# Kernel tuning notes

Hardware: AMD Instinct MI355X
Metric: run time of the kernel (lower is better)

The kernel has to match this reference:

```python
import jax, jax.numpy as jnp
import numpy as np

NUM_CLASSES = 1000
FEAT_DIM = 256
BATCH = 8192
MARGIN = 5.0
ALPHA = 1.0
BETA = 1.0


def setup_inputs() -> dict:
    key = jax.random.key(0)
    k1, k2, k3 = jax.random.split(key, 3)
    x = jax.random.normal(k1, (BATCH, FEAT_DIM), dtype=jnp.float32)
    labels = jax.random.randint(k2, (BATCH,), 0, NUM_CLASSES, dtype=jnp.int64)
    centers = jax.random.normal(k3, (NUM_CLASSES, FEAT_DIM), dtype=jnp.float32)
    return {"x": x, "labels": labels, "centers": centers}


def reference(x, labels, centers):
    # --- intra-class part ---
    # distmat_intra[i, j] = ||x_i||^2 + ||x_j||^2 - 2 x_i . x_j  (then relu + sqrt)
    mag = jnp.sum(x * x, axis=1)                      # (B,)
    sim = x @ x.T                                     # (B, B)
    d2 = mag[None, :] + mag[:, None] - 2.0 * sim      # (B, B)
    d = jnp.sqrt(jax.nn.relu(d2))                     # (B, B)

    # mask[i, j] = labels[i] == labels[j]; original gathers masked values per row,
    # clamps to [1e-12, 1e12], sorts descending and uses only the top-2 values.
    mask = labels[:, None] == labels[None, :]         # (B, B) bool
    vals = jnp.where(mask, jnp.clip(d, 1e-12, 1e12), -jnp.inf)
    top2, _ = jax.lax.top_k(vals.reshape(-1), 2)      # two largest intra-class dists
    k = 2.0
    loss_intra = k / (1.0 / top2[0] + 1.0 / top2[1])  # harmonic mean * k

    # --- inter-class part (faithful to original broadcasting) ---
    # distmat_inter[i, j] = 2 ||c_j||^2 - 2 c_i . c_j
    cmag = 2.0 * jnp.sum(centers * centers, axis=1)   # (C,)
    inter = cmag[None, :] - 2.0 * (centers @ centers.T)
    inter = jnp.clip(inter.reshape(-1), 1e-12, 1e12)
    loss_inter = jnp.clip(MARGIN - jnp.min(inter), 0.0, 1e6)

    return ALPHA * loss_intra + BETA * loss_inter
```

## Files before the change

kernel.cpp:

```cpp
#include <hip/hip_runtime.h>
#include <math.h>

#define BATCH 8192
#define FEAT  256
#define NCLS  1000

#define NGEMM  136
#define REPL   4
#define NINTRA (REPL*NCLS)
#define NBLK   (NGEMM + NINTRA)
#define ROWCAP 16
#define MEMCAP 96


__global__ __launch_bounds__(256) void k_main(const float* __restrict__ x,
                                              const int* __restrict__ labels,
                                              const float* __restrict__ centers,
                                              float* __restrict__ ws) {
    __shared__ __align__(16) char raw[18944];
    __shared__ float wred[4];
    __shared__ int cnt;
    int t = threadIdx.x;
    int lane = t & 63, w = t >> 6;

    if (blockIdx.x < NGEMM) {
        float (*As)[36] = reinterpret_cast<float(*)[36]>(raw);
        float (*Bs)[36] = reinterpret_cast<float(*)[36]>(raw + 9216);
        float* cmagI    = reinterpret_cast<float*>(raw + 18432);
        float* cmagJ    = reinterpret_cast<float*>(raw + 18688);

        int bi = 0, rem = blockIdx.x;
        while (rem >= 16 - bi) { rem -= 16 - bi; ++bi; }
        int bj = bi + rem;
        int i0 = bi * 64, j0 = bj * 64;

        for (int q = w; q < 64; q += 4) {
            int gi = i0 + q, gj = j0 + q;
            float sI = 0.0f, sJ = 0.0f;
            if (gi < NCLS) {
                float4 v = reinterpret_cast<const float4*>(centers + (size_t)gi * FEAT)[lane];
                sI = v.x * v.x + v.y * v.y + v.z * v.z + v.w * v.w;
            }
            if (gj < NCLS) {
                float4 v = reinterpret_cast<const float4*>(centers + (size_t)gj * FEAT)[lane];
                sJ = v.x * v.x + v.y * v.y + v.z * v.z + v.w * v.w;
            }
            #pragma unroll
            for (int o = 32; o > 0; o >>= 1) {
                sI += __shfl_xor(sI, o);
                sJ += __shfl_xor(sJ, o);
            }
            if (lane == 0) { cmagI[q] = 2.0f * sI; cmagJ[q] = 2.0f * sJ; }
        }

        int tx = t & 15, ty = t >> 4;
        float acc[4][4] = {{0.f}};
        for (int kk = 0; kk < FEAT; kk += 32) {
            #pragma unroll
            for (int e = t; e < 512; e += 256) {
                int row = e >> 3, q = e & 7;
                int col = kk + q * 4;
                int gi = i0 + row, gj = j0 + row;
                float4 av = (gi < NCLS)
                    ? *reinterpret_cast<const float4*>(centers + (size_t)gi * FEAT + col)
                    : make_float4(0.f, 0.f, 0.f, 0.f);
                float4 bv = (gj < NCLS)
                    ? *reinterpret_cast<const float4*>(centers + (size_t)gj * FEAT + col)
                    : make_float4(0.f, 0.f, 0.f, 0.f);
                *reinterpret_cast<float4*>(&As[row][q * 4]) = av;
                *reinterpret_cast<float4*>(&Bs[row][q * 4]) = bv;
            }
            __syncthreads();
            #pragma unroll
            for (int kc = 0; kc < 32; kc += 4) {
                float a[4][4], b[4][4];
                #pragma unroll
                for (int ii = 0; ii < 4; ++ii) {
                    float4 v = *reinterpret_cast<float4*>(&As[ty * 4 + ii][kc]);
                    a[ii][0] = v.x; a[ii][1] = v.y; a[ii][2] = v.z; a[ii][3] = v.w;
                }
                #pragma unroll
                for (int jj = 0; jj < 4; ++jj) {
                    float4 v = *reinterpret_cast<float4*>(&Bs[tx * 4 + jj][kc]);
                    b[jj][0] = v.x; b[jj][1] = v.y; b[jj][2] = v.z; b[jj][3] = v.w;
                }
                #pragma unroll
                for (int kq = 0; kq < 4; ++kq)
                    #pragma unroll
                    for (int ii = 0; ii < 4; ++ii)
                        #pragma unroll
                        for (int jj = 0; jj < 4; ++jj)
                            acc[ii][jj] += a[ii][kq] * b[jj][kq];
            }
            __syncthreads();
        }
        float lmin = 1e30f;
        #pragma unroll
        for (int jj = 0; jj < 4; ++jj) {
            int J = j0 + tx * 4 + jj;
            #pragma unroll
            for (int ii = 0; ii < 4; ++ii) {
                int I = i0 + ty * 4 + ii;
                if (I < NCLS && J < NCLS) {
                    float v1 = cmagJ[tx * 4 + jj] - 2.0f * acc[ii][jj];
                    v1 = fminf(fmaxf(v1, 1e-12f), 1e12f);
                    float v2 = cmagI[ty * 4 + ii] - 2.0f * acc[ii][jj];
                    v2 = fminf(fmaxf(v2, 1e-12f), 1e12f);
                    lmin = fminf(lmin, fminf(v1, v2));
                }
            }
        }
        #pragma unroll
        for (int o = 32; o > 0; o >>= 1) lmin = fminf(lmin, __shfl_xor(lmin, o));
        if (lane == 0) wred[w] = lmin;
        __syncthreads();
        if (t == 0) {
            float m = fminf(fminf(wred[0], wred[1]), fminf(wred[2], wred[3]));
            ws[blockIdx.x] = m;
        }
    } else {
        int bid = blockIdx.x - NGEMM;
        int c   = bid >> 2;
        int r   = bid & 3;
        float (*rowS)[256] = reinterpret_cast<float(*)[256]>(raw);
        int*   mem  = reinterpret_cast<int*>(raw + 16384);
        float* magS = reinterpret_cast<float*>(raw + 16768);

        if (t == 0) cnt = 0;
        __syncthreads();
        const int4* gl4 = reinterpret_cast<const int4*>(labels);
        #pragma unroll
        for (int k = 0; k < 8; ++k) {
            int4 lv = gl4[t + (k << 8)];
            int base = (t + (k << 8)) << 2;
            if (lv.x == c) { int p = atomicAdd(&cnt, 1); if (p < MEMCAP) mem[p] = base;     }
            if (lv.y == c) { int p = atomicAdd(&cnt, 1); if (p < MEMCAP) mem[p] = base + 1; }
            if (lv.z == c) { int p = atomicAdd(&cnt, 1); if (p < MEMCAP) mem[p] = base + 2; }
            if (lv.w == c) { int p = atomicAdd(&cnt, 1); if (p < MEMCAP) mem[p] = base + 3; }
        }
        __syncthreads();
        int n = cnt < MEMCAP ? cnt : MEMCAP;
        float vmax = 0.0f;
        if (n >= 2) {
            const float4* x4 = reinterpret_cast<const float4*>(x);
            for (int m = w; m < n; m += 4) {
                int row = mem[m];
                float4 v = x4[(size_t)row * 64 + lane];
                if (m < ROWCAP)
                    *reinterpret_cast<float4*>(&rowS[m][lane << 2]) = v;
                float s = v.x * v.x + v.y * v.y + v.z * v.z + v.w * v.w;
                #pragma unroll
                for (int o = 32; o > 0; o >>= 1) s += __shfl_xor(s, o);
                if (lane == 0) magS[m] = s;
            }
            __syncthreads();
            int npairs = n * (n - 1) / 2;
            for (int p = r * 4 + w; p < npairs; p += 16) {
                int a = 0, rem = p;
                while (rem >= n - 1 - a) { rem -= n - 1 - a; ++a; }
                int b = a + 1 + rem;
                float4 va = (a < ROWCAP)
                    ? *reinterpret_cast<float4*>(&rowS[a][lane << 2])
                    : x4[(size_t)mem[a] * 64 + lane];
                float4 vb = (b < ROWCAP)
                    ? *reinterpret_cast<float4*>(&rowS[b][lane << 2])
                    : x4[(size_t)mem[b] * 64 + lane];
                float s = va.x * vb.x + va.y * vb.y + va.z * vb.z + va.w * vb.w;
                #pragma unroll
                for (int o = 32; o > 0; o >>= 1) s += __shfl_xor(s, o);
                float d2 = magS[a] + magS[b] - 2.0f * s;
                float d  = sqrtf(fmaxf(d2, 0.0f));
                d = fminf(fmaxf(d, 1e-12f), 1e12f);
                vmax = fmaxf(vmax, d);
            }
        }
        if (lane == 0) wred[w] = vmax;
        __syncthreads();
        if (t == 0) {
            float m = fmaxf(fmaxf(wred[0], wred[1]), fmaxf(wred[2], wred[3]));
            ws[NGEMM + bid] = m;
        }
    }
}

__global__ __launch_bounds__(256) void k_final(const float* __restrict__ ws,
                                               float* __restrict__ out) {
    __shared__ float smx[4], smn[4];
    int t = threadIdx.x, lane = t & 63, w = t >> 6;
    float mn = 1e30f, mx = 0.0f;
    for (int i = t; i < NGEMM; i += 256)  mn = fminf(mn, ws[i]);
    for (int i = t; i < NINTRA; i += 256) mx = fmaxf(mx, ws[NGEMM + i]);
    #pragma unroll
    for (int o = 32; o > 0; o >>= 1) {
        mx = fmaxf(mx, __shfl_xor(mx, o));
        mn = fminf(mn, __shfl_xor(mn, o));
    }
    if (lane == 0) { smx[w] = mx; smn[w] = mn; }
    __syncthreads();
    if (t == 0) {
        mx = fmaxf(fmaxf(smx[0], smx[1]), fmaxf(smx[2], smx[3]));
        mn = fminf(fminf(smn[0], smn[1]), fminf(smn[2], smn[3]));
        float M = fmaxf(mx, 1e-12f);
        float r = 1.0f / M;
        float li2 = 2.0f / (r + r);
        float m = fminf(mn, 1e12f);
        float linter = fminf(fmaxf(5.0f - m, 0.0f), 1e6f);
        out[0] = li2 + linter;
    }
}

extern "C" void kernel_launch(void* const* d_in, const int* in_sizes, int n_in,
                              void* d_out, int out_size, void* d_ws, size_t ws_size,
                              hipStream_t stream) {
    const float* x       = (const float*)d_in[0];
    const int*   labels  = (const int*)d_in[1];
    const float* centers = (const float*)d_in[2];
    float*        ws     = (float*)d_ws;
    float*        out    = (float*)d_out;

    k_main<<<NBLK, 256, 0, stream>>>(x, labels, centers, ws);
    k_final<<<1, 256, 0, stream>>>(ws, out);
}
```

Baseline: 97.30 us.

## Shrink center-GEMM tiles to 32x32, halve intra replication, reorder block roles

The centers Gram GEMM now uses 32x32 tiles, which means 528 upper-triangular blocks instead of 136. Each thread computes a 2x2 output and loads are staged into a transposed shared-memory layout. Intra-class blocks now use 2 replicas per class instead of 4 and are placed first in the grid, with the GEMM blocks after them. The intent is to spread the GEMM across more CUs and cut redundant label scans in the intra blocks, at the cost of lower arithmetic intensity per GEMM block and more pair work per intra block.

```diff
diff --git a/kernel.cpp b/kernel.cpp
--- a/kernel.cpp
+++ b/kernel.cpp
@@ -5,123 +5,28 @@
 #define FEAT  256
 #define NCLS  1000
 
-#define NGEMM  136
-#define REPL   4
-#define NINTRA (REPL*NCLS)
-#define NBLK   (NGEMM + NINTRA)
-#define ROWCAP 16
-#define MEMCAP 96
+#define REPL    2
+#define NINTRA  (REPL*NCLS)
+#define NGEMM   528
+#define NBLK    (NINTRA + NGEMM)
+#define ROWCAP  16
+#define MEMCAP  96
 
 
 __global__ __launch_bounds__(256) void k_main(const float* __restrict__ x,
                                               const int* __restrict__ labels,
                                               const float* __restrict__ centers,
                                               float* __restrict__ ws) {
-    __shared__ __align__(16) char raw[18944];
+    __shared__ __align__(16) char raw[17152];
     __shared__ float wred[4];
     __shared__ int cnt;
     int t = threadIdx.x;
     int lane = t & 63, w = t >> 6;
 
-    if (blockIdx.x < NGEMM) {
-        float (*As)[36] = reinterpret_cast<float(*)[36]>(raw);
-        float (*Bs)[36] = reinterpret_cast<float(*)[36]>(raw + 9216);
-        float* cmagI    = reinterpret_cast<float*>(raw + 18432);
-        float* cmagJ    = reinterpret_cast<float*>(raw + 18688);
-
-        int bi = 0, rem = blockIdx.x;
-        while (rem >= 16 - bi) { rem -= 16 - bi; ++bi; }
-        int bj = bi + rem;
-        int i0 = bi * 64, j0 = bj * 64;
-
-        for (int q = w; q < 64; q += 4) {
-            int gi = i0 + q, gj = j0 + q;
-            float sI = 0.0f, sJ = 0.0f;
-            if (gi < NCLS) {
-                float4 v = reinterpret_cast<const float4*>(centers + (size_t)gi * FEAT)[lane];
-                sI = v.x * v.x + v.y * v.y + v.z * v.z + v.w * v.w;
-            }
-            if (gj < NCLS) {
-                float4 v = reinterpret_cast<const float4*>(centers + (size_t)gj * FEAT)[lane];
-                sJ = v.x * v.x + v.y * v.y + v.z * v.z + v.w * v.w;
-            }
-            #pragma unroll
-            for (int o = 32; o > 0; o >>= 1) {
-                sI += __shfl_xor(sI, o);
-                sJ += __shfl_xor(sJ, o);
-            }
-            if (lane == 0) { cmagI[q] = 2.0f * sI; cmagJ[q] = 2.0f * sJ; }
-        }
-
-        int tx = t & 15, ty = t >> 4;
-        float acc[4][4] = {{0.f}};
-        for (int kk = 0; kk < FEAT; kk += 32) {
-            #pragma unroll
-            for (int e = t; e < 512; e += 256) {
-                int row = e >> 3, q = e & 7;
-                int col = kk + q * 4;
-                int gi = i0 + row, gj = j0 + row;
-                float4 av = (gi < NCLS)
-                    ? *reinterpret_cast<const float4*>(centers + (size_t)gi * FEAT + col)
-                    : make_float4(0.f, 0.f, 0.f, 0.f);
-                float4 bv = (gj < NCLS)
-                    ? *reinterpret_cast<const float4*>(centers + (size_t)gj * FEAT + col)
-                    : make_float4(0.f, 0.f, 0.f, 0.f);
-                *reinterpret_cast<float4*>(&As[row][q * 4]) = av;
-                *reinterpret_cast<float4*>(&Bs[row][q * 4]) = bv;
-            }
-            __syncthreads();
-            #pragma unroll
-            for (int kc = 0; kc < 32; kc += 4) {
-                float a[4][4], b[4][4];
-                #pragma unroll
-                for (int ii = 0; ii < 4; ++ii) {
-                    float4 v = *reinterpret_cast<float4*>(&As[ty * 4 + ii][kc]);
-                    a[ii][0] = v.x; a[ii][1] = v.y; a[ii][2] = v.z; a[ii][3] = v.w;
-                }
-                #pragma unroll
-                for (int jj = 0; jj < 4; ++jj) {
-                    float4 v = *reinterpret_cast<float4*>(&Bs[tx * 4 + jj][kc]);
-                    b[jj][0] = v.x; b[jj][1] = v.y; b[jj][2] = v.z; b[jj][3] = v.w;
-                }
-                #pragma unroll
-                for (int kq = 0; kq < 4; ++kq)
-                    #pragma unroll
-                    for (int ii = 0; ii < 4; ++ii)
-                        #pragma unroll
-                        for (int jj = 0; jj < 4; ++jj)
-                            acc[ii][jj] += a[ii][kq] * b[jj][kq];
-            }
-            __syncthreads();
-        }
-        float lmin = 1e30f;
-        #pragma unroll
-        for (int jj = 0; jj < 4; ++jj) {
-            int J = j0 + tx * 4 + jj;
-            #pragma unroll
-            for (int ii = 0; ii < 4; ++ii) {
-                int I = i0 + ty * 4 + ii;
-                if (I < NCLS && J < NCLS) {
-                    float v1 = cmagJ[tx * 4 + jj] - 2.0f * acc[ii][jj];
-                    v1 = fminf(fmaxf(v1, 1e-12f), 1e12f);
-                    float v2 = cmagI[ty * 4 + ii] - 2.0f * acc[ii][jj];
-                    v2 = fminf(fmaxf(v2, 1e-12f), 1e12f);
-                    lmin = fminf(lmin, fminf(v1, v2));
-                }
-            }
-        }
-        #pragma unroll
-        for (int o = 32; o > 0; o >>= 1) lmin = fminf(lmin, __shfl_xor(lmin, o));
-        if (lane == 0) wred[w] = lmin;
-        __syncthreads();
-        if (t == 0) {
-            float m = fminf(fminf(wred[0], wred[1]), fminf(wred[2], wred[3]));
-            ws[blockIdx.x] = m;
-        }
-    } else {
-        int bid = blockIdx.x - NGEMM;
-        int c   = bid >> 2;
-        int r   = bid & 3;
+    if (blockIdx.x < NINTRA) {
+        int bid = blockIdx.x;
+        int c   = bid >> 1;
+        int r   = bid & 1;
         float (*rowS)[256] = reinterpret_cast<float(*)[256]>(raw);
         int*   mem  = reinterpret_cast<int*>(raw + 16384);
         float* magS = reinterpret_cast<float*>(raw + 16768);
@@ -155,7 +60,7 @@
             }
             __syncthreads();
             int npairs = n * (n - 1) / 2;
-            for (int p = r * 4 + w; p < npairs; p += 16) {
+            for (int p = r * 4 + w; p < npairs; p += 8) {
                 int a = 0, rem = p;
                 while (rem >= n - 1 - a) { rem -= n - 1 - a; ++a; }
                 int b = a + 1 + rem;
@@ -178,7 +83,89 @@
         __syncthreads();
         if (t == 0) {
             float m = fmaxf(fmaxf(wred[0], wred[1]), fmaxf(wred[2], wred[3]));
-            ws[NGEMM + bid] = m;
+            ws[bid] = m;
+        }
+    } else {
+        float (*As)[34] = reinterpret_cast<float(*)[34]>(raw);
+        float (*Bs)[34] = reinterpret_cast<float(*)[34]>(raw + 4352);
+        float* cmagI    = reinterpret_cast<float*>(raw + 8704);
+        float* cmagJ    = reinterpret_cast<float*>(raw + 8832);
+
+        int bi = 0, rem = blockIdx.x - NINTRA;
+        while (rem >= 32 - bi) { rem -= 32 - bi; ++bi; }
+        int bj = bi + rem;
+        int i0 = bi * 32, j0 = bj * 32;
+
+        for (int q = w; q < 32; q += 4) {
+            int gi = i0 + q, gj = j0 + q;
+            float sI = 0.0f, sJ = 0.0f;
+            if (gi < NCLS) {
+                float4 v = reinterpret_cast<const float4*>(centers + (size_t)gi * FEAT)[lane];
+                sI = v.x * v.x + v.y * v.y + v.z * v.z + v.w * v.w;
+            }
+            if (gj < NCLS) {
+                float4 v = reinterpret_cast<const float4*>(centers + (size_t)gj * FEAT)[lane];
+                sJ = v.x * v.x + v.y * v.y + v.z * v.z + v.w * v.w;
+            }
+            #pragma unroll
+            for (int o = 32; o > 0; o >>= 1) {
+                sI += __shfl_xor(sI, o);
+                sJ += __shfl_xor(sJ, o);
+            }
+            if (lane == 0) { cmagI[q] = 2.0f * sI; cmagJ[q] = 2.0f * sJ; }
+        }
+
+        int tx = t & 15, ty = t >> 4;
+        float acc[2][2] = {{0.f, 0.f}, {0.f, 0.f}};
+        for (int kk = 0; kk < FEAT; kk += 32) {
+            {
+                int row = t >> 3, q = t & 7;
+                int col = kk + q * 4;
+                int gi = i0 + row, gj = j0 + row;
+                float4 av = (gi < NCLS)
+                    ? *reinterpret_cast<const float4*>(centers + (size_t)gi * FEAT + col)
+                    : make_float4(0.f, 0.f, 0.f, 0.f);
+                float4 bv = (gj < NCLS)
+                    ? *reinterpret_cast<const float4*>(centers + (size_t)gj * FEAT + col)
+                    : make_float4(0.f, 0.f, 0.f, 0.f);
+                As[q * 4 + 0][row] = av.x; As[q * 4 + 1][row] = av.y;
+                As[q * 4 + 2][row] = av.z; As[q * 4 + 3][row] = av.w;
+                Bs[q * 4 + 0][row] = bv.x; Bs[q * 4 + 1][row] = bv.y;
+                Bs[q * 4 + 2][row] = bv.z; Bs[q * 4 + 3][row] = bv.w;
+            }
+            __syncthreads();
+            #pragma unroll
+            for (int k = 0; k < 32; ++k) {
+                float2 a2 = *reinterpret_cast<float2*>(&As[k][ty * 2]);
+                float2 b2 = *reinterpret_cast<float2*>(&Bs[k][tx * 2]);
+                acc[0][0] += a2.x * b2.x; acc[0][1] += a2.x * b2.y;
+                acc[1][0] += a2.y * b2.x; acc[1][1] += a2.y * b2.y;
+            }
+            __syncthreads();
+        }
+        float lmin = 1e30f;
+        #pragma unroll
+        for (int jj = 0; jj < 2; ++jj) {
+            int J = j0 + tx * 2 + jj;
+            #pragma unroll
+            for (int ii = 0; ii < 2; ++ii) {
+                int I = i0 + ty * 2 + ii;
+                if (I < NCLS && J < NCLS) {
+                    float v1 = cmagJ[tx * 2 + jj] - 2.0f * acc[ii][jj];
+                    v1 = fminf(fmaxf(v1, 1e-12f), 1e12f);
+                    float v2 = cmagI[ty * 2 + ii] - 2.0f * acc[ii][jj];
+                    v2 = fminf(fmaxf(v2, 1e-12f), 1e12f);
+                    lmin = fminf(lmin, fminf(v1, v2));
+                }
+            }
+        }
+        #pragma unroll
+        for (int o = 32; o > 0; o >>= 1) lmin = fminf(lmin, __shfl_xor(lmin, o));
+        if (lane == 0) wred[w] = lmin;
+        __syncthreads();
+        if (t == 0) {
+            float m = fminf(fminf(wred[0], wred[1]), fminf(wred[2], wred[3]));
+            ws[blockIdx.x] = m;
         }
     }
 }
@@ -188,8 +175,8 @@
     __shared__ float smx[4], smn[4];
     int t = threadIdx.x, lane = t & 63, w = t >> 6;
     float mn = 1e30f, mx = 0.0f;
-    for (int i = t; i < NGEMM; i += 256)  mn = fminf(mn, ws[i]);
-    for (int i = t; i < NINTRA; i += 256) mx = fmaxf(mx, ws[NGEMM + i]);
+    for (int i = t; i < NINTRA; i += 256) mx = fmaxf(mx, ws[i]);
+    for (int i = t; i < NGEMM; i += 256)  mn = fminf(mn, ws[NINTRA + i]);
     #pragma unroll
     for (int o = 32; o > 0; o >>= 1) {
         mx = fmaxf(mx, __shfl_xor(mx, o));
```

After: 101.7 us. +4.6%, slower.
